# Performance work log

Measured on AMD Instinct MI355X. Metric: run time of the kernel, lower is better.

The kernel has to match this reference:

```python
import jax, jax.numpy as jnp
import numpy as np

N_NODES = 50000
N_EDGES = 1600000
D_IN = 128
D_HID = 128
D_OUT = 128


def setup_inputs() -> dict:
    key = jax.random.key(0)
    k1, k2, k3, k4, k5, k6 = jax.random.split(key, 6)
    x = jax.random.normal(k1, (N_NODES, D_IN), dtype=jnp.float32)
    edge_index = jax.random.randint(k2, (2, N_EDGES), 0, N_NODES, dtype=jnp.int64)
    # glorot-ish init for GCNConv linear weights; bias zeros-like but randomized small
    W1 = jax.random.normal(k3, (D_IN, D_HID), dtype=jnp.float32) * (1.0 / np.sqrt(D_IN))
    b1 = jax.random.normal(k4, (D_HID,), dtype=jnp.float32) * 0.01
    W2 = jax.random.normal(k5, (D_HID, D_OUT), dtype=jnp.float32) * (1.0 / np.sqrt(D_HID))
    b2 = jax.random.normal(k6, (D_OUT,), dtype=jnp.float32) * 0.01
    return {"x": x, "edge_index": edge_index, "W1": W1, "b1": b1, "W2": W2, "b2": b2}


def gcn_conv(x, src, dst, W, b, n_nodes):
    # PyG GCNConv: add self-loops, symmetric normalization deg^-1/2, lin -> aggregate -> +bias
    loop = jnp.arange(n_nodes, dtype=src.dtype)
    s = jnp.concatenate([src, loop])  # [E+N]
    d = jnp.concatenate([dst, loop])  # [E+N]
    deg = jax.ops.segment_sum(jnp.ones_like(d, dtype=x.dtype), d, num_segments=n_nodes)
    dinv = jnp.where(deg > 0, jax.lax.rsqrt(deg), 0.0)
    norm = dinv[s] * dinv[d]  # [E+N]
    h = x @ W  # [N, F_out]
    msg = h[s] * norm[:, None]  # gather + scale: [E+N, F_out]
    out = jax.ops.segment_sum(msg, d, num_segments=n_nodes)  # scatter-add
    return out + b


def reference(x, edge_index, W1, b1, W2, b2):
    src, dst = edge_index[0], edge_index[1]
    h = gcn_conv(x, src, dst, W1, b1, N_NODES)
    h = jnp.where(h >= 0, h, 0.1 * h)  # LeakyReLU(0.1)
    h = gcn_conv(h, src, dst, W2, b2, N_NODES)
    return h.mean(axis=1)  # [N]
```

## Files before the change

kernel.cpp:

```cpp
#include <hip/hip_runtime.h>
#include <hip/hip_bf16.h>


#define N_NODES 50000
#define NPAD 50048
#define D 128
#define BK 196
#define CHUNK 4096

typedef unsigned int uint;
typedef unsigned short u16;
typedef __attribute__((ext_vector_type(8))) short short8;
typedef __attribute__((ext_vector_type(4))) float floatx4;

__device__ __forceinline__ u16 cvt_bf16(float f) {
    uint u = __float_as_uint(f);
    return (u16)((u + 0x7fffu + ((u >> 16) & 1u)) >> 16);
}
__device__ __forceinline__ uint pack_bf2(float a, float b) {
    return (uint)cvt_bf16(a) | ((uint)cvt_bf16(b) << 16);
}

__global__ void hist_w2m_kernel(const int* __restrict__ dst, uint* __restrict__ H,
                                const float* __restrict__ W2, const float* __restrict__ b2,
                                float* __restrict__ w2m, uint* __restrict__ counter,
                                int E, int CHN) {
    int t = threadIdx.x, c = blockIdx.x;
    if (c < CHN) {
        __shared__ uint h[BK];
        if (t < BK) h[t] = 0;
        __syncthreads();
        int e0 = c * CHUNK;
        for (int i = t; i < CHUNK; i += 256) {
            int e = e0 + i;
            if (e < E) atomicAdd(&h[dst[e] >> 8], 1u);
        }
        __syncthreads();
        if (t < BK) H[t * CHN + c] = h[t];
    } else {
        if (t < 128) {
            float s = 0.f;
            for (int j = 0; j < 128; j++) s += W2[t * 128 + j];
            w2m[t] = s * (1.0f / 128.0f);
        } else if (t == 128) {
            float s = 0.f;
            for (int j = 0; j < 128; j++) s += b2[j];
            w2m[128] = s * (1.0f / 128.0f);
        } else if (t == 129) {
            *counter = 0;
        }
    }
}

__global__ void scan_kernel(uint* __restrict__ H, uint* __restrict__ T, uint* __restrict__ B,
                            int* __restrict__ row, uint* __restrict__ counter,
                            int CHN, int E, int N) {
    __shared__ uint s[256];
    __shared__ uint ticket_sh;
    int t = threadIdx.x, b = blockIdx.x;
    uint carry = 0;
    for (int base = 0; base < CHN; base += 256) {
        int idx = base + t;
        uint v = (idx < CHN) ? H[b * CHN + idx] : 0u;
        s[t] = v;
        __syncthreads();
#pragma unroll
        for (int off = 1; off < 256; off <<= 1) {
            uint u = (t >= off) ? s[t - off] : 0u;
            __syncthreads();
            s[t] += u;
            __syncthreads();
        }
        if (idx < CHN) H[b * CHN + idx] = carry + s[t] - v;
        carry += s[255];
        __syncthreads();
    }
    if (t == 0) {
        atomicExch(&T[b], carry);
        __threadfence();
        ticket_sh = atomicAdd(counter, 1);
    }
    __syncthreads();
    if (ticket_sh == (uint)(gridDim.x - 1)) {
        __threadfence();
        uint v = (t < BK) ? atomicAdd(&T[t], 0u) : 0u;
        s[t] = v;
        __syncthreads();
#pragma unroll
        for (int off = 1; off < 256; off <<= 1) {
            uint u = (t >= off) ? s[t - off] : 0u;
            __syncthreads();
            s[t] += u;
            __syncthreads();
        }
        if (t < BK) B[t] = s[t] - v;
        if (t == 0) { B[BK] = (uint)E; row[N] = E; }
    }
}

__global__ void scatter_kernel(const int* __restrict__ src, const int* __restrict__ dst,
                               const uint* __restrict__ H, const uint* __restrict__ B,
                               uint* __restrict__ EB, int E, int CHN) {
    __shared__ uint cur[BK];
    int t = threadIdx.x, c = blockIdx.x;
    if (t < BK) cur[t] = B[t] + H[t * CHN + c];
    __syncthreads();
    int e0 = c * CHUNK;
    for (int i = t; i < CHUNK; i += 256) {
        int e = e0 + i;
        if (e < E) {
            int d = dst[e];
            uint slot = atomicAdd(&cur[d >> 8], 1u);
            EB[slot] = ((uint)(d & 255) << 16) | (uint)src[e];
        }
    }
}

#define WT_STRIDE 136
union SortGemmSmem {
    struct { uint cnt[256], s[256], cur[256]; } sort;
    u16 wt[128 * WT_STRIDE];
};
__global__ __launch_bounds__(256) void sortgemm_kernel(
    const uint* __restrict__ EB, const uint* __restrict__ B,
    int* __restrict__ row, float* __restrict__ dinv, u16* __restrict__ esrc,
    const float* __restrict__ A, const float* __restrict__ W,
    uint* __restrict__ G32, int N, int M) {
    __shared__ SortGemmSmem sm;
    int t = threadIdx.x;

    if (blockIdx.x < BK) {
        int b = blockIdx.x;
        uint base = B[b], ne = B[b + 1] - base;
        sm.sort.cnt[t] = 0;
        __syncthreads();
        for (uint i = t; i < ne; i += 256) atomicAdd(&sm.sort.cnt[EB[base + i] >> 16], 1u);
        __syncthreads();
        uint c = sm.sort.cnt[t];
        sm.sort.s[t] = c;
        __syncthreads();
#pragma unroll
        for (int off = 1; off < 256; off <<= 1) {
            uint u = (t >= off) ? sm.sort.s[t - off] : 0u;
            __syncthreads();
            sm.sort.s[t] += u;
            __syncthreads();
        }
        uint p = sm.sort.s[t] - c;
        int v = (b << 8) + t;
        if (v < N) {
            row[v] = (int)(base + p);
            dinv[v] = rsqrtf((float)(c + 1u));
        }
        sm.sort.cur[t] = base + p;
        __syncthreads();
        for (uint i = t; i < ne; i += 256) {
            uint u = EB[base + i];
            uint slot = atomicAdd(&sm.sort.cur[u >> 16], 1u);
            esrc[slot] = (u16)(u & 0xffffu);
        }
    } else {
        int bid = blockIdx.x - BK;
        for (int i = t; i < 128 * 128; i += 256) {
            int k = i >> 7, n = i & 127;
            sm.wt[n * WT_STRIDE + k] = cvt_bf16(W[i]);
        }
        __syncthreads();

        int wave = t >> 6, lane = t & 63;
        int m = lane & 15, quad = lane >> 4;
        int rowa = bid * 64 + wave * 16 + m;
        int rowc = rowa < M ? rowa : M - 1;
        const float* Arow = A + (long)rowc * D;

        short8 afrag[4];
#pragma unroll
        for (int kt = 0; kt < 4; kt++) {
            int k0 = kt * 32 + quad * 8;
            float4 f0 = *(const float4*)(Arow + k0);
            float4 f1 = *(const float4*)(Arow + k0 + 4);
            short8 af;
            af[0] = (short)cvt_bf16(f0.x); af[1] = (short)cvt_bf16(f0.y);
            af[2] = (short)cvt_bf16(f0.z); af[3] = (short)cvt_bf16(f0.w);
            af[4] = (short)cvt_bf16(f1.x); af[5] = (short)cvt_bf16(f1.y);
            af[6] = (short)cvt_bf16(f1.z); af[7] = (short)cvt_bf16(f1.w);
            afrag[kt] = af;
        }

        int orow0 = bid * 64 + wave * 16;
        for (int n0 = 0; n0 < 128; n0 += 16) {
            floatx4 acc = {0.f, 0.f, 0.f, 0.f};
#pragma unroll
            for (int kt = 0; kt < 4; kt++) {
                short8 bf = *(const short8*)(sm.wt + (n0 + m) * WT_STRIDE + kt * 32 + quad * 8);
                acc = __builtin_amdgcn_mfma_f32_16x16x32_bf16(afrag[kt], bf, acc, 0, 0, 0);
            }
#pragma unroll
            for (int r = 0; r < 4; r++) {
                float val = acc[r];
                float oth = __shfl_xor(val, 1, 64);
                int orow = orow0 + quad * 4 + r;
                if (orow < M && (m & 1) == 0) {
                    int c = n0 + m;
                    G32[(long)(c >> 5) * NPAD * 16 + (long)orow * 16 + ((c & 31) >> 1)]
                        = pack_bf2(val, oth);
                }
            }
        }
    }
}

__global__ __launch_bounds__(256) void gather_q2_kernel(
    const int* __restrict__ row, const u16* __restrict__ esrc,
    const uint* __restrict__ g16, const float* __restrict__ dinv,
    const float* __restrict__ b1, const float* __restrict__ w2m,
    float* __restrict__ partial, int N) {
    int b = blockIdx.x;
    int slot = b & 7;
    int q = slot >> 1;
    int wave = threadIdx.x >> 6;
    int lane = threadIdx.x & 63;
    int grp = lane >> 4;
    int g = lane & 15;
    int chain = g >> 2, p = g & 3;
    int v = (b >> 3) * 32 + (slot & 1) * 16 + wave * 4 + grp;
    if (v >= N) return;

    const uint4* gq = (const uint4*)(g16 + (long)q * NPAD * 16);
    float dvv = dinv[v];
    float acc[8];
#pragma unroll
    for (int i = 0; i < 8; i++) acc[i] = 0.f;

#define ACC4(u, wgt) {                                                   \
    acc[0] += (wgt) * __uint_as_float((u).x << 16);                      \
    acc[1] += (wgt) * __uint_as_float((u).x & 0xffff0000u);              \
    acc[2] += (wgt) * __uint_as_float((u).y << 16);                      \
    acc[3] += (wgt) * __uint_as_float((u).y & 0xffff0000u);              \
    acc[4] += (wgt) * __uint_as_float((u).z << 16);                      \
    acc[5] += (wgt) * __uint_as_float((u).z & 0xffff0000u);              \
    acc[6] += (wgt) * __uint_as_float((u).w << 16);                      \
    acc[7] += (wgt) * __uint_as_float((u).w & 0xffff0000u); }

    if (chain == 0) {
        uint4 u = gq[(long)v * 4 + p];
        ACC4(u, dvv)
    }
    int jb = (int)__builtin_nontemporal_load(&row[v]);
    int je = (int)__builtin_nontemporal_load(&row[v + 1]);
    int j = jb + chain;
    if (j < je) {
        int s0 = (int)__builtin_nontemporal_load(&esrc[j]);
        float w0 = dinv[s0];
        uint4 u0 = gq[(long)s0 * 4 + p];
        j += 4;
        while (j < je) {
            int s1 = (int)__builtin_nontemporal_load(&esrc[j]);
            float w1 = dinv[s1];
            uint4 u1 = gq[(long)s1 * 4 + p];
            j += 4;
            ACC4(u0, w0)
            u0 = u1; w0 = w1;
        }
        ACC4(u0, w0)
    }
#undef ACC4

#pragma unroll
    for (int i = 0; i < 8; i++) {
        acc[i] += __shfl_xor(acc[i], 4, 64);
        acc[i] += __shfl_xor(acc[i], 8, 64);
    }

    const float2* bp = (const float2*)b1;
    const float2* wp = (const float2*)w2m;
    float s = 0.f;
#pragma unroll
    for (int k = 0; k < 4; k++) {
        float2 bb = bp[q * 16 + p * 4 + k];
        float2 wm = wp[q * 16 + p * 4 + k];
        float t0 = dvv * acc[2 * k]     + bb.x; t0 = t0 >= 0.f ? t0 : 0.1f * t0;
        float t1 = dvv * acc[2 * k + 1] + bb.y; t1 = t1 >= 0.f ? t1 : 0.1f * t1;
        s += t0 * wm.x + t1 * wm.y;
    }
    s += __shfl_xor(s, 1, 64);
    s += __shfl_xor(s, 2, 64);
    if (g == 0) partial[q * NPAD + v] = s;
}

__global__ void mg_kernel(const float* __restrict__ partial, const float* __restrict__ dinv,
                          float* __restrict__ mg, int N) {
    int v = blockIdx.x * blockDim.x + threadIdx.x;
    if (v >= N) return;
    mg[v] = dinv[v] * (partial[v] + partial[NPAD + v] +
                       partial[2 * NPAD + v] + partial[3 * NPAD + v]);
}

__global__ void out_kernel(const int* __restrict__ row, const u16* __restrict__ esrc,
                           const float* __restrict__ mg, const float* __restrict__ dinv,
                           const float* __restrict__ w2m, float* __restrict__ out, int N) {
    int v = blockIdx.x * blockDim.x + threadIdx.x;
    if (v >= N) return;
    float acc = mg[v];
    int jb = row[v], je = row[v + 1];
    int j = jb;
    for (; j + 8 <= je; j += 8) {
        acc += mg[esrc[j]] + mg[esrc[j + 1]] + mg[esrc[j + 2]] + mg[esrc[j + 3]] +
               mg[esrc[j + 4]] + mg[esrc[j + 5]] + mg[esrc[j + 6]] + mg[esrc[j + 7]];
    }
    for (; j < je; j++) acc += mg[esrc[j]];
    out[v] = dinv[v] * acc + w2m[128];
}

extern "C" void kernel_launch(void* const* d_in, const int* in_sizes, int n_in,
                              void* d_out, int out_size, void* d_ws, size_t ws_size,
                              hipStream_t stream) {
    const float* x  = (const float*)d_in[0];
    const int* ei   = (const int*)d_in[1];
    const float* W1 = (const float*)d_in[2];
    const float* b1 = (const float*)d_in[3];
    const float* W2 = (const float*)d_in[4];
    const float* b2 = (const float*)d_in[5];
    float* out = (float*)d_out;

    const int N = N_NODES;
    const int E = in_sizes[1] / 2;
    const int* src = ei;
    const int* dst = ei + E;
    const int CHN = (E + CHUNK - 1) / CHUNK;
    const int nblocks = (N + 255) / 256;

    float*    dinv    = (float*)d_ws;
    int*      row     = (int*)(dinv + NPAD);
    uint*     B       = (uint*)(row + NPAD + 16);
    float*    w2m     = (float*)(B + 256);
    float*    mg      = w2m + 256;
    uint*     T       = (uint*)(mg + NPAD);
    uint*     counter = T + 256;
    float*    partial = (float*)(counter + 16);
    uint*     g16u    = (uint*)(partial + 4 * NPAD);
    u16*      esrc    = (u16*)(g16u + (long)NPAD * 64);
    uint*     H       = (uint*)(esrc + E);
    uint*     EB      = H + BK * CHN;

    hist_w2m_kernel<<<CHN + 1, 256, 0, stream>>>(dst, H, W2, b2, w2m, counter, E, CHN);
    scan_kernel<<<BK, 256, 0, stream>>>(H, T, B, row, counter, CHN, E, N);
    scatter_kernel<<<CHN, 256, 0, stream>>>(src, dst, H, B, EB, E, CHN);
    sortgemm_kernel<<<BK + (N + 63) / 64, 256, 0, stream>>>(EB, B, row, dinv, esrc,
                                                            x, W1, g16u, N, N);
    gather_q2_kernel<<<((N + 31) / 32) * 8, 256, 0, stream>>>(row, esrc, g16u, dinv,
                                                              b1, w2m, partial, N);
    mg_kernel<<<nblocks, 256, 0, stream>>>(partial, dinv, mg, N);
    out_kernel<<<nblocks, 256, 0, stream>>>(row, esrc, mg, dinv, w2m, out, N);
}
```

Baseline: 228.8 us.

## Parallelize W2 row-mean across waves and deepen gather prefetch to two stages

The W2/b2 column-mean work, previously done serially by single threads in one extra block, is spread over 33 extra blocks with one wave per row and a shuffle reduction, so it no longer serializes the tail of the histogram kernel. The neighbor-gather loop now keeps two loads in flight per chain instead of one, to hide more gather latency. Nontemporal load hints on row/esrc are also dropped. The deeper prefetch raises register use and may reduce occupancy.

```diff
diff --git a/kernel.cpp b/kernel.cpp
--- a/kernel.cpp
+++ b/kernel.cpp
@@ -38,16 +38,20 @@
         __syncthreads();
         if (t < BK) H[t * CHN + c] = h[t];
     } else {
-        if (t < 128) {
-            float s = 0.f;
-            for (int j = 0; j < 128; j++) s += W2[t * 128 + j];
-            w2m[t] = s * (1.0f / 128.0f);
-        } else if (t == 128) {
-            float s = 0.f;
-            for (int j = 0; j < 128; j++) s += b2[j];
-            w2m[128] = s * (1.0f / 128.0f);
-        } else if (t == 129) {
-            *counter = 0;
+        int wave = t >> 6, lane = t & 63;
+        int k = (c - CHN) * 4 + wave;
+        if (k < 128) {
+            float s = W2[k * 128 + lane] + W2[k * 128 + 64 + lane];
+#pragma unroll
+            for (int off = 32; off > 0; off >>= 1) s += __shfl_down(s, off, 64);
+            if (lane == 0) w2m[k] = s * (1.0f / 128.0f);
+        } else if (k == 128) {
+            float s = b2[lane] + b2[lane + 64];
+#pragma unroll
+            for (int off = 32; off > 0; off >>= 1) s += __shfl_down(s, off, 64);
+            if (lane == 0) w2m[128] = s * (1.0f / 128.0f);
+        } else if (k == 129) {
+            if (lane == 0) *counter = 0;
         }
     }
 }
@@ -210,7 +214,7 @@
     }
 }
 
-__global__ __launch_bounds__(256) void gather_q2_kernel(
+__global__ __launch_bounds__(256) void gather_q3_kernel(
     const int* __restrict__ row, const u16* __restrict__ esrc,
     const uint* __restrict__ g16, const float* __restrict__ dinv,
     const float* __restrict__ b1, const float* __restrict__ w2m,
@@ -246,23 +250,32 @@
         uint4 u = gq[(long)v * 4 + p];
         ACC4(u, dvv)
     }
-    int jb = (int)__builtin_nontemporal_load(&row[v]);
-    int je = (int)__builtin_nontemporal_load(&row[v + 1]);
+    int jb = row[v], je = row[v + 1];
     int j = jb + chain;
     if (j < je) {
-        int s0 = (int)__builtin_nontemporal_load(&esrc[j]);
+        int s0 = esrc[j];
         float w0 = dinv[s0];
         uint4 u0 = gq[(long)s0 * 4 + p];
-        j += 4;
-        while (j < je) {
-            int s1 = (int)__builtin_nontemporal_load(&esrc[j]);
+        int j1 = j + 4;
+        if (j1 < je) {
+            int s1 = esrc[j1];
             float w1 = dinv[s1];
             uint4 u1 = gq[(long)s1 * 4 + p];
-            j += 4;
+            int j2 = j1 + 4;
+            while (j2 < je) {
+                int s2 = esrc[j2];
+                float w2 = dinv[s2];
+                uint4 u2 = gq[(long)s2 * 4 + p];
+                j2 += 4;
+                ACC4(u0, w0)
+                u0 = u1; w0 = w1;
+                u1 = u2; w1 = w2;
+            }
             ACC4(u0, w0)
-            u0 = u1; w0 = w1;
-        }
-        ACC4(u0, w0)
+            ACC4(u1, w1)
+        } else {
+            ACC4(u0, w0)
+        }
     }
 #undef ACC4
 
@@ -343,12 +356,12 @@
     uint*     H       = (uint*)(esrc + E);
     uint*     EB      = H + BK * CHN;
 
-    hist_w2m_kernel<<<CHN + 1, 256, 0, stream>>>(dst, H, W2, b2, w2m, counter, E, CHN);
+    hist_w2m_kernel<<<CHN + 33, 256, 0, stream>>>(dst, H, W2, b2, w2m, counter, E, CHN);
     scan_kernel<<<BK, 256, 0, stream>>>(H, T, B, row, counter, CHN, E, N);
     scatter_kernel<<<CHN, 256, 0, stream>>>(src, dst, H, B, EB, E, CHN);
     sortgemm_kernel<<<BK + (N + 63) / 64, 256, 0, stream>>>(EB, B, row, dinv, esrc,
                                                             x, W1, g16u, N, N);
-    gather_q2_kernel<<<((N + 31) / 32) * 8, 256, 0, stream>>>(row, esrc, g16u, dinv,
+    gather_q3_kernel<<<((N + 31) / 32) * 8, 256, 0, stream>>>(row, esrc, g16u, dinv,
                                                               b1, w2m, partial, N);
     mg_kernel<<<nblocks, 256, 0, stream>>>(partial, dinv, mg, N);
     out_kernel<<<nblocks, 256, 0, stream>>>(row, esrc, mg, dinv, w2m, out, N);
```

New measurement: 206.7 us. 1.11x faster.
